# Kernel optimization log

Hardware: AMD Instinct MI355X
Metric: run time of the kernel (lower is better)

The kernel has to match this reference:

```python
import jax, jax.numpy as jnp
import numpy as np

N_NODES = 50000
N_EDGES = 800000
D_IN = 64
D_OUT = 64


def setup_inputs() -> dict:
    key = jax.random.key(0)
    k1, k2, k3 = jax.random.split(key, 3)
    x = jax.random.normal(k1, (N_NODES, D_IN), dtype=jnp.float32)
    edge_index = jax.random.randint(k2, (2, N_EDGES), 0, N_NODES, dtype=jnp.int64)
    # xavier_uniform for weight [in, out]
    limit = np.sqrt(6.0 / (D_IN + D_OUT)).astype(np.float32)
    weight = jax.random.uniform(k3, (D_IN, D_OUT), dtype=jnp.float32, minval=-limit, maxval=limit)
    bias = jnp.zeros((D_OUT,), dtype=jnp.float32)
    return {"x": x, "edge_index": edge_index, "weight": weight, "bias": bias}


def reference(x, edge_index, weight, bias):
    n = x.shape[0]
    # add self loops
    loops = jnp.arange(n, dtype=edge_index.dtype)
    row = jnp.concatenate([edge_index[0], loops])  # [E+N]
    col = jnp.concatenate([edge_index[1], loops])  # [E+N]
    # degree over row (as in torch_geometric degree(row, N))
    deg = jax.ops.segment_sum(jnp.ones_like(row, dtype=x.dtype), row, num_segments=n)
    deg_inv_sqrt = jnp.where(deg > 0, jax.lax.rsqrt(deg), jnp.zeros_like(deg))
    norm = deg_inv_sqrt[row] * deg_inv_sqrt[col]  # [E+N]
    h = x @ weight  # [N, D_OUT]
    # gather-scale-scatter: out[col] += h[row] * norm
    out = jax.ops.segment_sum(h[row] * norm[:, None], col, num_segments=n)
    return out + bias
```

## Files before the change

kernel.cpp:

```cpp
#include <hip/hip_runtime.h>
#include <hip/hip_bf16.h>


constexpr int N_NODES = 50000;
constexpr int N_EDGES = 800000;
constexpr int D = 64;
constexpr int NB_SCAN = (N_NODES + 255) / 256;

constexpr int B_SLICE = 64;
constexpr int SLICE = N_EDGES / B_SLICE;
constexpr int PACK8 = N_NODES / 4;
constexpr int QUAR = N_NODES / 4;
constexpr int NB_GEMM = (N_NODES + 63) / 64;

static __device__ __forceinline__ unsigned short f2bf(float f) {
    unsigned u = __float_as_uint(f);
    unsigned r = (u + 0x7fffu + ((u >> 16) & 1u)) >> 16;
    return (unsigned short)r;
}
static __device__ __forceinline__ float bf2f(unsigned short s) {
    return __uint_as_float((unsigned)s << 16);
}

__global__ __launch_bounds__(1024) void hist_priv_kernel(const int* __restrict__ ei,
                                                         unsigned* __restrict__ bh) {
    __shared__ unsigned loc[PACK8];
    int b = blockIdx.x;
    int s = b & (B_SLICE - 1);
    const int* arr = (b < B_SLICE) ? ei : ei + N_EDGES;
    for (int w = threadIdx.x; w < PACK8; w += 1024) loc[w] = 0;
    __syncthreads();
    const int* p = arr + s * SLICE;
    for (int i = threadIdx.x; i < SLICE; i += 1024) {
        int k = p[i];
        atomicAdd(&loc[k >> 2], 1u << (8 * (k & 3)));
    }
    __syncthreads();
    unsigned* dst = bh + (size_t)b * PACK8;
    for (int w = threadIdx.x; w < PACK8; w += 1024) dst[w] = loc[w];
}

__global__ __launch_bounds__(256, 4) void fused_reduce_gemm(
        const unsigned* __restrict__ bh,
        float* __restrict__ dis,
        int* __restrict__ offs_local,
        int* __restrict__ partials,
        unsigned char* __restrict__ bs8,
        const float* __restrict__ x, const float* __restrict__ W,
        unsigned short* __restrict__ hs) {
    __shared__ union {
        struct { float Xs[64][68]; float Ws[64][64]; } g;
        int s[256];
    } lds;
    const int b = blockIdx.x;
    const int t = threadIdx.x;

    if (b < NB_GEMM) {
        int n0 = b * 64;

        const float4* W4 = (const float4*)W;
        float4* Ws4 = (float4*)lds.g.Ws;
#pragma unroll
        for (int i = 0; i < 4; ++i) Ws4[t + i * 256] = W4[t + i * 256];

        const float4* x4 = (const float4*)(x + (size_t)n0 * D);
#pragma unroll
        for (int i = 0; i < 4; ++i) {
            int f = t + i * 256;
            int r = f >> 4, c = (f & 15) << 2;
            float4 v = make_float4(0.f, 0.f, 0.f, 0.f);
            if (n0 + r < N_NODES) v = x4[f];
            lds.g.Xs[r][c] = v.x; lds.g.Xs[r][c + 1] = v.y;
            lds.g.Xs[r][c + 2] = v.z; lds.g.Xs[r][c + 3] = v.w;
        }
        __syncthreads();

        int tx = t & 15, ty = t >> 4;
        float acc[4][4] = {};
#pragma unroll 8
        for (int k = 0; k < D; ++k) {
            float a[4], bb[4];
#pragma unroll
            for (int i = 0; i < 4; ++i) a[i] = lds.g.Xs[ty * 4 + i][k];
#pragma unroll
            for (int jj = 0; jj < 4; ++jj) bb[jj] = lds.g.Ws[k][tx * 4 + jj];
#pragma unroll
            for (int i = 0; i < 4; ++i)
#pragma unroll
                for (int jj = 0; jj < 4; ++jj)
                    acc[i][jj] = fmaf(a[i], bb[jj], acc[i][jj]);
        }

#pragma unroll
        for (int i = 0; i < 4; ++i) {
            int r = ty * 4 + i;
            if (n0 + r < N_NODES) {
                ushort4 v;
                v.x = f2bf(acc[i][0]); v.y = f2bf(acc[i][1]);
                v.z = f2bf(acc[i][2]); v.w = f2bf(acc[i][3]);
                *(ushort4*)(hs + (size_t)(n0 + r) * D + tx * 4) = v;
            }
        }
    } else {
        const int rb = b - NB_GEMM;
        int i = rb * 256 + t;
        unsigned cl = 0;
        if (i < N_NODES) {
            const int w = i >> 2;
            const unsigned sh = 8 * (i & 3);
            const unsigned* prow = bh + w;
            unsigned dl = 0;
#pragma unroll
            for (int g = 0; g < 4; ++g) {
                unsigned vr[16];
#pragma unroll
                for (int k = 0; k < 16; ++k) vr[k] = prow[(size_t)(g * 16 + k) * PACK8];
#pragma unroll
                for (int k = 0; k < 16; ++k) dl += (vr[k] >> sh) & 0xffu;
            }
            dis[i] = rsqrtf((float)dl + 1.0f);
            const unsigned* pcol = bh + (size_t)B_SLICE * PACK8 + w;
#pragma unroll
            for (int g = 0; g < 4; ++g) {
                unsigned vr[16];
#pragma unroll
                for (int k = 0; k < 16; ++k) vr[k] = pcol[(size_t)(g * 16 + k) * PACK8];
#pragma unroll
                for (int k = 0; k < 16; ++k) {
                    bs8[(size_t)(g * 16 + k) * N_NODES + i] = (unsigned char)cl;
                    cl += (vr[k] >> sh) & 0xffu;
                }
            }
        }
        lds.s[t] = (int)cl;
        __syncthreads();
        for (int d = 1; d < 256; d <<= 1) {
            int u = (t >= d) ? lds.s[t - d] : 0;
            __syncthreads();
            lds.s[t] += u;
            __syncthreads();
        }
        if (i < N_NODES) offs_local[i] = lds.s[t] - (int)cl;
        if (t == 255) partials[rb] = lds.s[t];
    }
}

__global__ __launch_bounds__(1024) void bucket_det_kernel(const int* __restrict__ ei,
                                                          const int* __restrict__ offs_local,
                                                          const int* __restrict__ partials,
                                                          const unsigned char* __restrict__ bs8,
                                                          int* __restrict__ csr,
                                                          int* __restrict__ offs) {
    __shared__ unsigned pos[QUAR / 4];
    __shared__ int pref[256];
    const int t = threadIdx.x;

    if (t < 256) pref[t] = (t < NB_SCAN) ? partials[t] : 0;
    __syncthreads();
    for (int d = 1; d < 256; d <<= 1) {
        int u = 0;
        if (t < 256 && t >= d) u = pref[t - d];
        __syncthreads();
        if (t < 256) pref[t] += u;
        __syncthreads();
    }
    if (t < 256) {
        int inc = pref[t];
        int own = (t < NB_SCAN) ? partials[t] : 0;
        pref[t] = inc - own;
    }
    __syncthreads();

    const int s = blockIdx.x >> 2;
    const int q = blockIdx.x & 3;
    const int c0 = q * QUAR;

    const unsigned* rel32 = (const unsigned*)(bs8 + (size_t)s * N_NODES + c0);
    for (int w = t; w < QUAR / 4; w += 1024) pos[w] = rel32[w];

    if (s == 0) {
        const int* olq = offs_local + c0;
        for (int w = t; w < QUAR; w += 1024) {
            int node = c0 + w;
            offs[node] = pref[node >> 8] + olq[w];
        }
        if (q == 3 && t == 0) offs[N_NODES] = N_EDGES;
    }
    __syncthreads();

    const int* rowp = ei + s * SLICE;
    const int* colp = ei + N_EDGES + s * SLICE;
    for (int i = t; i < SLICE; i += 1024) {
        int c = colp[i];
        unsigned cc = (unsigned)(c - c0);
        if (cc < (unsigned)QUAR) {
            int base = pref[c >> 8] + offs_local[c];
            unsigned old = atomicAdd(&pos[cc >> 2], 1u << (8 * (cc & 3)));
            unsigned rel = (old >> (8 * (cc & 3))) & 0xffu;
            csr[base + (int)rel] = rowp[i];
        }
    }
}

__global__ __launch_bounds__(256) void gather_kernel(const int* __restrict__ offs,
                                                     const int* __restrict__ csr,
                                                     const unsigned short* __restrict__ hs,
                                                     const float* __restrict__ dis,
                                                     const float* __restrict__ bias,
                                                     float* __restrict__ out) {
    int wave = threadIdx.x >> 6;
    int j = threadIdx.x & 63;
    int n = blockIdx.x * 4 + wave;
    if (n >= N_NODES) return;

    float dn = dis[n];
    float a[8];
    a[0] = dn * bf2f(hs[(size_t)n * D + j]);
#pragma unroll
    for (int k = 1; k < 8; ++k) a[k] = 0.f;

    int beg = __builtin_amdgcn_readfirstlane(offs[n]);
    int m   = __builtin_amdgcn_readfirstlane(offs[n + 1]) - beg;
    const int* p = csr + beg;

    int i = 0;
    for (; i + 16 <= m; i += 16) {
        int r[16];
        float dr[16];
        float v[16];
#pragma unroll
        for (int k = 0; k < 16; ++k) r[k] = p[i + k];
#pragma unroll
        for (int k = 0; k < 16; ++k) dr[k] = dis[r[k]];
#pragma unroll
        for (int k = 0; k < 16; ++k) v[k] = bf2f(hs[(size_t)r[k] * D + j]);
#pragma unroll
        for (int k = 0; k < 16; ++k) a[k & 7] = fmaf(v[k], dr[k], a[k & 7]);
    }
    for (; i + 4 <= m; i += 4) {
        int r0 = p[i], r1 = p[i + 1], r2 = p[i + 2], r3 = p[i + 3];
        a[0] = fmaf(bf2f(hs[(size_t)r0 * D + j]), dis[r0], a[0]);
        a[1] = fmaf(bf2f(hs[(size_t)r1 * D + j]), dis[r1], a[1]);
        a[2] = fmaf(bf2f(hs[(size_t)r2 * D + j]), dis[r2], a[2]);
        a[3] = fmaf(bf2f(hs[(size_t)r3 * D + j]), dis[r3], a[3]);
    }
    for (; i < m; ++i) {
        int r0 = p[i];
        a[1] = fmaf(bf2f(hs[(size_t)r0 * D + j]), dis[r0], a[1]);
    }
    float tot = ((a[0] + a[1]) + (a[2] + a[3])) + ((a[4] + a[5]) + (a[6] + a[7]));
    out[(size_t)n * D + j] = fmaf(dn, tot, bias[j]);
}


__global__ __launch_bounds__(256, 4) void gemm_plain_kernel(const float* __restrict__ x,
                                                            const float* __restrict__ W,
                                                            unsigned short* __restrict__ hs) {
    __shared__ float Xs[64][68];
    __shared__ float Ws[64][64];
    int t = threadIdx.x;
    int n0 = blockIdx.x * 64;

    const float4* W4 = (const float4*)W;
    float4* Ws4 = (float4*)Ws;
#pragma unroll
    for (int i = 0; i < 4; ++i) Ws4[t + i * 256] = W4[t + i * 256];

    const float4* x4 = (const float4*)(x + (size_t)n0 * D);
#pragma unroll
    for (int i = 0; i < 4; ++i) {
        int f = t + i * 256;
        int r = f >> 4, c = (f & 15) << 2;
        float4 v = make_float4(0.f, 0.f, 0.f, 0.f);
        if (n0 + r < N_NODES) v = x4[f];
        Xs[r][c] = v.x; Xs[r][c + 1] = v.y; Xs[r][c + 2] = v.z; Xs[r][c + 3] = v.w;
    }
    __syncthreads();

    int tx = t & 15, ty = t >> 4;
    float acc[4][4] = {};
#pragma unroll 8
    for (int k = 0; k < D; ++k) {
        float a[4], bb[4];
#pragma unroll
        for (int i = 0; i < 4; ++i) a[i] = Xs[ty * 4 + i][k];
#pragma unroll
        for (int jj = 0; jj < 4; ++jj) bb[jj] = Ws[k][tx * 4 + jj];
#pragma unroll
        for (int i = 0; i < 4; ++i)
#pragma unroll
            for (int jj = 0; jj < 4; ++jj)
                acc[i][jj] = fmaf(a[i], bb[jj], acc[i][jj]);
    }

#pragma unroll
    for (int i = 0; i < 4; ++i) {
        int r = ty * 4 + i;
        if (n0 + r < N_NODES) {
            ushort4 v;
            v.x = f2bf(acc[i][0]); v.y = f2bf(acc[i][1]);
            v.z = f2bf(acc[i][2]); v.w = f2bf(acc[i][3]);
            *(ushort4*)(hs + (size_t)(n0 + r) * D + tx * 4) = v;
        }
    }
}

__global__ void histf_kernel(const int* __restrict__ row, const int* __restrict__ col,
                             int* __restrict__ degi, int* __restrict__ cnt) {
    int e = blockIdx.x * blockDim.x + threadIdx.x;
    if (e < N_EDGES) {
        atomicAdd(&degi[row[e]], 1);
        atomicAdd(&cnt[col[e]], 1);
    }
}

__global__ void disf_kernel(int* __restrict__ degi) {
    int i = blockIdx.x * blockDim.x + threadIdx.x;
    if (i < N_NODES) {
        float d = (float)degi[i] + 1.0f;
        ((float*)degi)[i] = rsqrtf(d);
    }
}

__global__ void block_scan_kernel(const int* __restrict__ cnt, int* __restrict__ offs,
                                  int* __restrict__ partials) {
    __shared__ int s[256];
    int t = threadIdx.x;
    int i = blockIdx.x * 256 + t;
    int v = (i < N_NODES) ? cnt[i] : 0;
    s[t] = v;
    __syncthreads();
    for (int d = 1; d < 256; d <<= 1) {
        int u = (t >= d) ? s[t - d] : 0;
        __syncthreads();
        s[t] += u;
        __syncthreads();
    }
    if (i < N_NODES) offs[i] = s[t] - v;
    if (t == 255) partials[blockIdx.x] = s[t];
}

__global__ void scan_partials_kernel(int* __restrict__ partials) {
    __shared__ int s[256];
    int t = threadIdx.x;
    int v = (t < NB_SCAN) ? partials[t] : 0;
    s[t] = v;
    __syncthreads();
    for (int d = 1; d < 256; d <<= 1) {
        int u = (t >= d) ? s[t - d] : 0;
        __syncthreads();
        s[t] += u;
        __syncthreads();
    }
    if (t < NB_SCAN) partials[t] = s[t] - v;
}

__global__ void add_off_kernel(int* __restrict__ offs, const int* __restrict__ partials) {
    int i = blockIdx.x * 256 + threadIdx.x;
    if (i < N_NODES) offs[i] += partials[blockIdx.x];
    if (i == 0) offs[N_NODES] = N_EDGES;
}

__global__ void bucket_fb_kernel(const int* __restrict__ row, const int* __restrict__ col,
                                 const int* __restrict__ offs, int* __restrict__ cur,
                                 int* __restrict__ csr) {
    int e = blockIdx.x * blockDim.x + threadIdx.x;
    if (e < N_EDGES) {
        int c = col[e];
        int pos = offs[c] + atomicAdd(&cur[c], 1);
        csr[pos] = row[e];
    }
}


extern "C" void kernel_launch(void* const* d_in, const int* in_sizes, int n_in,
                              void* d_out, int out_size, void* d_ws, size_t ws_size,
                              hipStream_t stream) {
    const float* x    = (const float*)d_in[0];
    const int*   ei   = (const int*)d_in[1];
    const float* W    = (const float*)d_in[2];
    const float* bias = (const float*)d_in[3];
    float* out = (float*)d_out;

    char* ws = (char*)d_ws;
    float*          dis      = (float*)(ws + 0);
    int*            offs     = (int*)(ws + 200000);
    int*            offs_loc = (int*)(ws + 400064);
    int*            cur      = (int*)(ws + 600064);
    int*            partials = (int*)(ws + 800064);
    int*            csr      = (int*)(ws + 801088);
    unsigned short* hs       = (unsigned short*)(ws + 4001088);
    unsigned*       bh       = (unsigned*)(ws + 10401088);
    unsigned char*  bs8      = (unsigned char*)(ws + 16801088);

    const size_t WS_NEEDED = 20001088;

    if (ws_size >= WS_NEEDED) {
        hist_priv_kernel<<<2 * B_SLICE, 1024, 0, stream>>>(ei, bh);
        fused_reduce_gemm<<<NB_GEMM + NB_SCAN, 256, 0, stream>>>(bh, dis, offs_loc,
                                                                 partials, bs8, x, W, hs);
        bucket_det_kernel<<<4 * B_SLICE, 1024, 0, stream>>>(ei, offs_loc, partials, bs8,
                                                            csr, offs);
        gather_kernel<<<(N_NODES + 3) / 4, 256, 0, stream>>>(offs, csr, hs, dis, bias, out);
    } else {
        const int* row = ei;
        const int* col = ei + N_EDGES;
        int* degi = (int*)dis;
        int* cntf = offs_loc;
        hipMemsetAsync(ws, 0, 800064, stream);
        histf_kernel<<<(N_EDGES + 255) / 256, 256, 0, stream>>>(row, col, degi, cntf);
        disf_kernel<<<(N_NODES + 255) / 256, 256, 0, stream>>>(degi);
        block_scan_kernel<<<NB_SCAN, 256, 0, stream>>>(cntf, offs, partials);
        scan_partials_kernel<<<1, 256, 0, stream>>>(partials);
        add_off_kernel<<<NB_SCAN, 256, 0, stream>>>(offs, partials);
        gemm_plain_kernel<<<(N_NODES + 63) / 64, 256, 0, stream>>>(x, W, hs);
        bucket_fb_kernel<<<(N_EDGES + 255) / 256, 256, 0, stream>>>(row, col, offs, cur, csr);
        gather_kernel<<<(N_NODES + 3) / 4, 256, 0, stream>>>(offs, csr, hs, dis, bias, out);
    }
}
```

Baseline: 135.9 us.

## Prescale GEMM output by source norm and compute degrees via global packed atomics

The GEMM epilogue now multiplies each row of h by deg^-1/2 of its source node before storing it as bf16. This removes the per-edge random dis[row] load and the multiply from the gather loop. Row degrees are now counted directly into a global packed 8-bit array with atomics, replacing the per-slice private histograms that the reduce step had to sum. The reduce and GEMM kernel is rebuilt with 1024-thread blocks: column-slice prefix work is split across four groups, and each block runs four GEMM tiles. The trade-offs are global atomic contention, an added memset, and applying the bf16 rounding after the scaling.

```diff
diff --git a/kernel.cpp b/kernel.cpp
--- a/kernel.cpp
+++ b/kernel.cpp
@@ -11,7 +11,6 @@
 constexpr int SLICE = N_EDGES / B_SLICE;
 constexpr int PACK8 = N_NODES / 4;
 constexpr int QUAR = N_NODES / 4;
-constexpr int NB_GEMM = (N_NODES + 63) / 64;
 
 static __device__ __forceinline__ unsigned short f2bf(float f) {
     unsigned u = __float_as_uint(f);
@@ -23,67 +22,127 @@
 }
 
 __global__ __launch_bounds__(1024) void hist_priv_kernel(const int* __restrict__ ei,
-                                                         unsigned* __restrict__ bh) {
+                                                         unsigned* __restrict__ bh,
+                                                         unsigned* __restrict__ degp8) {
     __shared__ unsigned loc[PACK8];
     int b = blockIdx.x;
-    int s = b & (B_SLICE - 1);
-    const int* arr = (b < B_SLICE) ? ei : ei + N_EDGES;
-    for (int w = threadIdx.x; w < PACK8; w += 1024) loc[w] = 0;
-    __syncthreads();
-    const int* p = arr + s * SLICE;
-    for (int i = threadIdx.x; i < SLICE; i += 1024) {
-        int k = p[i];
-        atomicAdd(&loc[k >> 2], 1u << (8 * (k & 3)));
-    }
-    __syncthreads();
-    unsigned* dst = bh + (size_t)b * PACK8;
-    for (int w = threadIdx.x; w < PACK8; w += 1024) dst[w] = loc[w];
-}
-
-__global__ __launch_bounds__(256, 4) void fused_reduce_gemm(
+    if (b < B_SLICE) {
+        const int* p = ei + b * SLICE;
+        for (int i = threadIdx.x; i < SLICE; i += 1024) {
+            int k = p[i];
+            atomicAdd(&degp8[k >> 2], 1u << (8 * (k & 3)));
+        }
+    } else {
+        int s = b - B_SLICE;
+        for (int w = threadIdx.x; w < PACK8; w += 1024) loc[w] = 0;
+        __syncthreads();
+        const int* p = ei + N_EDGES + s * SLICE;
+        for (int i = threadIdx.x; i < SLICE; i += 1024) {
+            int k = p[i];
+            atomicAdd(&loc[k >> 2], 1u << (8 * (k & 3)));
+        }
+        __syncthreads();
+        unsigned* dst = bh + (size_t)b * PACK8;
+        for (int w = threadIdx.x; w < PACK8; w += 1024) dst[w] = loc[w];
+    }
+}
+
+struct FLds {
+    union {
+        struct { int colp[4][256]; int s[256]; } r;
+        struct { float Xs[4][64][68]; float Ws[64][64]; } g;
+    } u;
+};
+
+__global__ __launch_bounds__(1024) void fused_rg_kernel(
         const unsigned* __restrict__ bh,
+        const unsigned* __restrict__ degp8,
         float* __restrict__ dis,
         int* __restrict__ offs_local,
         int* __restrict__ partials,
         unsigned char* __restrict__ bs8,
-        const float* __restrict__ x, const float* __restrict__ W,
+        const float* __restrict__ x,
+        const float* __restrict__ W,
         unsigned short* __restrict__ hs) {
-    __shared__ union {
-        struct { float Xs[64][68]; float Ws[64][64]; } g;
-        int s[256];
-    } lds;
+    __shared__ FLds L;
+    const int t = threadIdx.x;
     const int b = blockIdx.x;
-    const int t = threadIdx.x;
-
-    if (b < NB_GEMM) {
-        int n0 = b * 64;
-
-        const float4* W4 = (const float4*)W;
-        float4* Ws4 = (float4*)lds.g.Ws;
-#pragma unroll
-        for (int i = 0; i < 4; ++i) Ws4[t + i * 256] = W4[t + i * 256];
-
+
+    if (b < NB_SCAN) {
+        const int nl = t & 255;
+        const int g = t >> 8;
+        const int i = b * 256 + nl;
+
+        unsigned lp[16];
+        if (i < N_NODES) {
+            const int w = i >> 2;
+            const unsigned sh = 8 * (i & 3);
+            const unsigned* pcol = bh + (size_t)(B_SLICE + g * 16) * PACK8 + w;
+            unsigned vc[16];
+#pragma unroll
+            for (int k = 0; k < 16; ++k) vc[k] = pcol[(size_t)k * PACK8];
+            unsigned c = 0;
+#pragma unroll
+            for (int k = 0; k < 16; ++k) { lp[k] = c; c += (vc[k] >> sh) & 0xffu; }
+            L.u.r.colp[g][nl] = (int)c;
+        } else {
+            L.u.r.colp[g][nl] = 0;
+        }
+        __syncthreads();
+
+        if (i < N_NODES) {
+            int base = 0;
+#pragma unroll
+            for (int gg = 0; gg < 4; ++gg) if (gg < g) base += L.u.r.colp[gg][nl];
+#pragma unroll
+            for (int k = 0; k < 16; ++k)
+                bs8[(size_t)(g * 16 + k) * N_NODES + i] = (unsigned char)(base + (int)lp[k]);
+        }
+        if (g == 0)
+            L.u.r.s[nl] = L.u.r.colp[0][nl] + L.u.r.colp[1][nl] +
+                          L.u.r.colp[2][nl] + L.u.r.colp[3][nl];
+        __syncthreads();
+
+        for (int d = 1; d < 256; d <<= 1) {
+            int u = (t < 256 && t >= d) ? L.u.r.s[t - d] : 0;
+            __syncthreads();
+            if (t < 256) L.u.r.s[t] += u;
+            __syncthreads();
+        }
+        if (g == 0 && i < N_NODES) {
+            int tot = L.u.r.colp[0][nl] + L.u.r.colp[1][nl] +
+                      L.u.r.colp[2][nl] + L.u.r.colp[3][nl];
+            offs_local[i] = L.u.r.s[nl] - tot;
+        }
+        if (t == 255) partials[b] = L.u.r.s[255];
+    } else {
+        const int grp = t >> 8, t256 = t & 255;
+        const int tb = (b - NB_SCAN) * 4 + grp;
+        const int n0 = tb * 64;
+
+        ((float4*)L.u.g.Ws)[t] = ((const float4*)W)[t];
+
+        float (*Xs)[68] = L.u.g.Xs[grp];
         const float4* x4 = (const float4*)(x + (size_t)n0 * D);
 #pragma unroll
         for (int i = 0; i < 4; ++i) {
-            int f = t + i * 256;
+            int f = t256 + i * 256;
             int r = f >> 4, c = (f & 15) << 2;
             float4 v = make_float4(0.f, 0.f, 0.f, 0.f);
             if (n0 + r < N_NODES) v = x4[f];
-            lds.g.Xs[r][c] = v.x; lds.g.Xs[r][c + 1] = v.y;
-            lds.g.Xs[r][c + 2] = v.z; lds.g.Xs[r][c + 3] = v.w;
-        }
-        __syncthreads();
-
-        int tx = t & 15, ty = t >> 4;
+            Xs[r][c] = v.x; Xs[r][c + 1] = v.y; Xs[r][c + 2] = v.z; Xs[r][c + 3] = v.w;
+        }
+        __syncthreads();
+
+        int tx = t256 & 15, ty = t256 >> 4;
         float acc[4][4] = {};
 #pragma unroll 8
         for (int k = 0; k < D; ++k) {
             float a[4], bb[4];
 #pragma unroll
-            for (int i = 0; i < 4; ++i) a[i] = lds.g.Xs[ty * 4 + i][k];
-#pragma unroll
-            for (int jj = 0; jj < 4; ++jj) bb[jj] = lds.g.Ws[k][tx * 4 + jj];
+            for (int i = 0; i < 4; ++i) a[i] = Xs[ty * 4 + i][k];
+#pragma unroll
+            for (int jj = 0; jj < 4; ++jj) bb[jj] = L.u.g.Ws[k][tx * 4 + jj];
 #pragma unroll
             for (int i = 0; i < 4; ++i)
 #pragma unroll
@@ -94,54 +153,18 @@
 #pragma unroll
         for (int i = 0; i < 4; ++i) {
             int r = ty * 4 + i;
-            if (n0 + r < N_NODES) {
+            int node = n0 + r;
+            if (node < N_NODES) {
+                unsigned dw = degp8[node >> 2];
+                float deg = (float)((dw >> (8 * (node & 3))) & 0xffu);
+                float dr = rsqrtf(deg + 1.0f);
+                if (tx == 0) dis[node] = dr;
                 ushort4 v;
-                v.x = f2bf(acc[i][0]); v.y = f2bf(acc[i][1]);
-                v.z = f2bf(acc[i][2]); v.w = f2bf(acc[i][3]);
-                *(ushort4*)(hs + (size_t)(n0 + r) * D + tx * 4) = v;
+                v.x = f2bf(acc[i][0] * dr); v.y = f2bf(acc[i][1] * dr);
+                v.z = f2bf(acc[i][2] * dr); v.w = f2bf(acc[i][3] * dr);
+                *(ushort4*)(hs + (size_t)node * D + tx * 4) = v;
             }
         }
-    } else {
-        const int rb = b - NB_GEMM;
-        int i = rb * 256 + t;
-        unsigned cl = 0;
-        if (i < N_NODES) {
-            const int w = i >> 2;
-            const unsigned sh = 8 * (i & 3);
-            const unsigned* prow = bh + w;
-            unsigned dl = 0;
-#pragma unroll
-            for (int g = 0; g < 4; ++g) {
-                unsigned vr[16];
-#pragma unroll
-                for (int k = 0; k < 16; ++k) vr[k] = prow[(size_t)(g * 16 + k) * PACK8];
-#pragma unroll
-                for (int k = 0; k < 16; ++k) dl += (vr[k] >> sh) & 0xffu;
-            }
-            dis[i] = rsqrtf((float)dl + 1.0f);
-            const unsigned* pcol = bh + (size_t)B_SLICE * PACK8 + w;
-#pragma unroll
-            for (int g = 0; g < 4; ++g) {
-                unsigned vr[16];
-#pragma unroll
-                for (int k = 0; k < 16; ++k) vr[k] = pcol[(size_t)(g * 16 + k) * PACK8];
-#pragma unroll
-                for (int k = 0; k < 16; ++k) {
-                    bs8[(size_t)(g * 16 + k) * N_NODES + i] = (unsigned char)cl;
-                    cl += (vr[k] >> sh) & 0xffu;
-                }
-            }
-        }
-        lds.s[t] = (int)cl;
-        __syncthreads();
-        for (int d = 1; d < 256; d <<= 1) {
-            int u = (t >= d) ? lds.s[t - d] : 0;
-            __syncthreads();
-            lds.s[t] += u;
-            __syncthreads();
-        }
-        if (i < N_NODES) offs_local[i] = lds.s[t] - (int)cl;
-        if (t == 255) partials[rb] = lds.s[t];
     }
 }
 
@@ -213,9 +236,8 @@
     int n = blockIdx.x * 4 + wave;
     if (n >= N_NODES) return;
 
-    float dn = dis[n];
     float a[8];
-    a[0] = dn * bf2f(hs[(size_t)n * D + j]);
+    a[0] = bf2f(hs[(size_t)n * D + j]);
 #pragma unroll
     for (int k = 1; k < 8; ++k) a[k] = 0.f;
 
@@ -226,35 +248,30 @@
     int i = 0;
     for (; i + 16 <= m; i += 16) {
         int r[16];
-        float dr[16];
         float v[16];
 #pragma unroll
         for (int k = 0; k < 16; ++k) r[k] = p[i + k];
 #pragma unroll
-        for (int k = 0; k < 16; ++k) dr[k] = dis[r[k]];
-#pragma unroll
         for (int k = 0; k < 16; ++k) v[k] = bf2f(hs[(size_t)r[k] * D + j]);
 #pragma unroll
-        for (int k = 0; k < 16; ++k) a[k & 7] = fmaf(v[k], dr[k], a[k & 7]);
+        for (int k = 0; k < 16; ++k) a[k & 7] += v[k];
     }
     for (; i + 4 <= m; i += 4) {
         int r0 = p[i], r1 = p[i + 1], r2 = p[i + 2], r3 = p[i + 3];
-        a[0] = fmaf(bf2f(hs[(size_t)r0 * D + j]), dis[r0], a[0]);
-        a[1] = fmaf(bf2f(hs[(size_t)r1 * D + j]), dis[r1], a[1]);
-        a[2] = fmaf(bf2f(hs[(size_t)r2 * D + j]), dis[r2], a[2]);
-        a[3] = fmaf(bf2f(hs[(size_t)r3 * D + j]), dis[r3], a[3]);
-    }
-    for (; i < m; ++i) {
-        int r0 = p[i];
-        a[1] = fmaf(bf2f(hs[(size_t)r0 * D + j]), dis[r0], a[1]);
-    }
+        a[0] += bf2f(hs[(size_t)r0 * D + j]);
+        a[1] += bf2f(hs[(size_t)r1 * D + j]);
+        a[2] += bf2f(hs[(size_t)r2 * D + j]);
+        a[3] += bf2f(hs[(size_t)r3 * D + j]);
+    }
+    for (; i < m; ++i) a[1] += bf2f(hs[(size_t)p[i] * D + j]);
     float tot = ((a[0] + a[1]) + (a[2] + a[3])) + ((a[4] + a[5]) + (a[6] + a[7]));
-    out[(size_t)n * D + j] = fmaf(dn, tot, bias[j]);
+    out[(size_t)n * D + j] = fmaf(dis[n], tot, bias[j]);
 }
 
 
 __global__ __launch_bounds__(256, 4) void gemm_plain_kernel(const float* __restrict__ x,
                                                             const float* __restrict__ W,
+                                                            const float* __restrict__ dis,
                                                             unsigned short* __restrict__ hs) {
     __shared__ float Xs[64][68];
     __shared__ float Ws[64][64];
@@ -297,9 +314,10 @@
     for (int i = 0; i < 4; ++i) {
         int r = ty * 4 + i;
         if (n0 + r < N_NODES) {
+            float dr = dis[n0 + r];
             ushort4 v;
-            v.x = f2bf(acc[i][0]); v.y = f2bf(acc[i][1]);
-            v.z = f2bf(acc[i][2]); v.w = f2bf(acc[i][3]);
+            v.x = f2bf(acc[i][0] * dr); v.y = f2bf(acc[i][1] * dr);
+            v.z = f2bf(acc[i][2] * dr); v.w = f2bf(acc[i][3] * dr);
             *(ushort4*)(hs + (size_t)(n0 + r) * D + tx * 4) = v;
         }
     }
@@ -386,6 +404,7 @@
     float*          dis      = (float*)(ws + 0);
     int*            offs     = (int*)(ws + 200000);
     int*            offs_loc = (int*)(ws + 400064);
+    unsigned*       degp8    = (unsigned*)(ws + 600064);
     int*            cur      = (int*)(ws + 600064);
     int*            partials = (int*)(ws + 800064);
     int*            csr      = (int*)(ws + 801088);
@@ -396,9 +415,10 @@
     const size_t WS_NEEDED = 20001088;
 
     if (ws_size >= WS_NEEDED) {
-        hist_priv_kernel<<<2 * B_SLICE, 1024, 0, stream>>>(ei, bh);
-        fused_reduce_gemm<<<NB_GEMM + NB_SCAN, 256, 0, stream>>>(bh, dis, offs_loc,
-                                                                 partials, bs8, x, W, hs);
+        hipMemsetAsync(degp8, 0, PACK8 * 4, stream);
+        hist_priv_kernel<<<2 * B_SLICE, 1024, 0, stream>>>(ei, bh, degp8);
+        fused_rg_kernel<<<NB_SCAN + NB_SCAN, 1024, 0, stream>>>(bh, degp8, dis, offs_loc,
+                                                                partials, bs8, x, W, hs);
         bucket_det_kernel<<<4 * B_SLICE, 1024, 0, stream>>>(ei, offs_loc, partials, bs8,
                                                             csr, offs);
         gather_kernel<<<(N_NODES + 3) / 4, 256, 0, stream>>>(offs, csr, hs, dis, bias, out);
@@ -413,7 +433,7 @@
         block_scan_kernel<<<NB_SCAN, 256, 0, stream>>>(cntf, offs, partials);
         scan_partials_kernel<<<1, 256, 0, stream>>>(partials);
         add_off_kernel<<<NB_SCAN, 256, 0, stream>>>(offs, partials);
-        gemm_plain_kernel<<<(N_NODES + 63) / 64, 256, 0, stream>>>(x, W, hs);
+        gemm_plain_kernel<<<(N_NODES + 63) / 64, 256, 0, stream>>>(x, W, dis, hs);
         bucket_fb_kernel<<<(N_EDGES + 255) / 256, 256, 0, stream>>>(row, col, offs, cur, csr);
         gather_kernel<<<(N_NODES + 3) / 4, 256, 0, stream>>>(offs, csr, hs, dis, bias, out);
     }
```

Result: slower. 170.4 us (+25.4%).
